# Optimization experiments

Hardware: AMD Instinct MI355X
Metric: run time of the kernel (lower is better)

## Reference

```python
import jax, jax.numpy as jnp
import numpy as np

DIM_E, DIM_M, DIM_C = 1024, 64, 128
B, N = 4, 4096


def setup_inputs() -> dict:
    key = jax.random.key(0)
    ks = jax.random.split(key, 10)
    s = 1.0 / np.sqrt(DIM_E + DIM_C)
    return {
        "e": jax.random.normal(ks[0], (B, N, DIM_E), jnp.float32),
        "m": jax.random.normal(ks[1], (B, N, DIM_M), jnp.float32),
        "c": jax.random.normal(ks[2], (B, N, DIM_C), jnp.float32),
        "l": jax.random.uniform(ks[3], (B, N), jnp.float32),
        "Wq": jax.random.uniform(ks[4], (DIM_E + DIM_C, DIM_E), jnp.float32, -s, s),
        "bq": jax.random.uniform(ks[5], (DIM_E,), jnp.float32, -s, s),
        "Wk": jax.random.uniform(ks[6], (DIM_E + DIM_C, DIM_E), jnp.float32, -s, s),
        "bk": jax.random.uniform(ks[7], (DIM_E,), jnp.float32, -s, s),
        "Wv": jax.random.uniform(ks[8], (DIM_E + DIM_C, DIM_E), jnp.float32, -s, s),
        "bv": jax.random.uniform(ks[9], (DIM_E,), jnp.float32, -s, s),
    }


def reference(e, m, c, l, Wq, bq, Wk, bk, Wv, bv):
    x = jnp.concatenate([e, c], axis=-1)                       # [B,N,De+Dc]
    q = jnp.einsum('bnd,df->bnf', x, Wq) + bq                  # [B,N,De]
    k = jnp.einsum('bnd,df->bnf', x, Wk) + bk
    v = jnp.einsum('bnd,df->bnf', x, Wv) + bv
    scale = 1.0 / jnp.sqrt(jnp.asarray(q.shape[-1], q.dtype))
    attn_scores = jnp.einsum('bqd,bkd->bqk', q, k) * scale     # [B,N,N]
    membrane_mask = jnp.einsum('bqm,bkm->bqk', m, m)           # [B,N,N]
    lifespan_mask = l[:, :, None] * l[:, None, :]              # [B,N,N]
    adaptive_scores = attn_scores * membrane_mask * lifespan_mask
    attn_weights = jax.nn.softmax(adaptive_scores, axis=-1)
    h_tilde = jnp.einsum('bqk,bkd->bqd', attn_weights, v)      # [B,N,De]
    e_new = e + h_tilde
    return (e_new, h_tilde)
```

## Files before the change

kernel.cpp:

```cpp
#include <hip/hip_runtime.h>
#include <hip/hip_bf16.h>

#define DE 1024
#define DM 64
#define DC 128
#define DX 1152
#define NB 4
#define NN 4096
#define NT 16384

typedef _Float16 f16;
typedef _Float16 f16x4 __attribute__((ext_vector_type(4)));
typedef _Float16 f16x8 __attribute__((ext_vector_type(8)));
typedef float f32x4 __attribute__((ext_vector_type(4)));

__device__ __forceinline__ void g2l16(const void* g, void* l) {
  __builtin_amdgcn_global_load_lds(
      (const __attribute__((address_space(1))) unsigned int*)(unsigned long long)g,
      (__attribute__((address_space(3))) unsigned int*)(unsigned int)(unsigned long long)l,
      16, 0, 0);
}

__global__ void build_x_kernel(const float* __restrict__ e, const float* __restrict__ c,
                               f16* __restrict__ Xb) {
  const int total = NT * DX / 4;
  for (int i = blockIdx.x * blockDim.x + threadIdx.x; i < total; i += gridDim.x * blockDim.x) {
    int idx = i * 4;
    int r = idx / DX, col = idx - r * DX;
    float4 v;
    if (col < DE) v = *(const float4*)(e + (long)r * DE + col);
    else          v = *(const float4*)(c + (long)r * DC + (col - DE));
    f16x4 o = { (f16)v.x, (f16)v.y, (f16)v.z, (f16)v.w };
    *(f16x4*)(Xb + (long)idx) = o;
  }
}

__global__ void conv_f16_kernel(const float* __restrict__ in, f16* __restrict__ out, int total4) {
  for (int i = blockIdx.x * blockDim.x + threadIdx.x; i < total4; i += gridDim.x * blockDim.x) {
    float4 v = *(const float4*)(in + (long)i * 4);
    f16x4 o = { (f16)v.x, (f16)v.y, (f16)v.z, (f16)v.w };
    *(f16x4*)(out + (long)i * 4) = o;
  }
}

__global__ void transpose_w_kernel(const float* __restrict__ in, f16* __restrict__ out) {
  __shared__ float tile[32][33];
  int c0 = blockIdx.x * 32, r0 = blockIdx.y * 32;
  int x = threadIdx.x, y = threadIdx.y;
#pragma unroll
  for (int i = 0; i < 4; ++i)
    tile[y + 8 * i][x] = in[(long)(r0 + y + 8 * i) * DE + (c0 + x)];
  __syncthreads();
#pragma unroll
  for (int i = 0; i < 4; ++i)
    out[(long)(c0 + y + 8 * i) * DX + (r0 + x)] = (f16)tile[x][y + 8 * i];
}

__device__ __forceinline__ void mm_loop(const f16* __restrict__ A, const f16* __restrict__ B,
                                        int lda, int ldb, int K,
                                        f16* lA, f16* lB, f32x4 (&acc)[4][4]) {
  const int t = threadIdx.x;
  const int lane = t & 63;
  const int wid = t >> 6;
  const int wr = (wid >> 1) * 64, wc = (wid & 1) * 64;
  const int fr = lane & 15, fq = lane >> 4;
  for (int k0 = 0; k0 < K; k0 += 32) {
    __syncthreads();
#pragma unroll
    for (int it = 0; it < 2; ++it) {
      int byteoff = it * 4096 + t * 16;
      int row = byteoff >> 6;
      int ke = (byteoff & 63) >> 1;
      g2l16(A + (long)row * lda + k0 + ke, lA + (byteoff >> 1));
      g2l16(B + (long)row * ldb + k0 + ke, lB + (byteoff >> 1));
    }
    __syncthreads();
    f16x8 af[4], bfr[4];
#pragma unroll
    for (int i = 0; i < 4; ++i) {
      af[i]  = *(const f16x8*)(lA + (wr + i * 16 + fr) * 32 + fq * 8);
      bfr[i] = *(const f16x8*)(lB + (wc + i * 16 + fr) * 32 + fq * 8);
    }
#pragma unroll
    for (int m = 0; m < 4; ++m)
#pragma unroll
      for (int n = 0; n < 4; ++n)
        acc[m][n] = __builtin_amdgcn_mfma_f32_16x16x32_f16(af[m], bfr[n], acc[m][n], 0, 0, 0);
  }
}

#define GEMM_PRE()                                                    \
  __shared__ __attribute__((aligned(16))) f16 lA[128 * 32], lB[128 * 32]; \
  f32x4 acc[4][4];                                                    \
  _Pragma("unroll") for (int m = 0; m < 4; ++m)                       \
  _Pragma("unroll") for (int n = 0; n < 4; ++n)                       \
      acc[m][n] = (f32x4){0.f, 0.f, 0.f, 0.f};

#define EPI_IDX()                                                     \
  const int lane = threadIdx.x & 63, wid = threadIdx.x >> 6;          \
  const int wr = (wid >> 1) * 64, wc = (wid & 1) * 64;                \
  const int fr = lane & 15, fq = lane >> 4;

__global__ __launch_bounds__(256) void gemm_qk_kernel(
    const f16* __restrict__ Xb, const f16* __restrict__ Wt,
    const float* __restrict__ bq, const float* __restrict__ bk,
    f16* __restrict__ qb, f16* __restrict__ kb) {
  GEMM_PRE();
  const int row0 = blockIdx.x * 128, col0 = blockIdx.y * 128;
  mm_loop(Xb + (long)row0 * DX, Wt + (long)col0 * DX, DX, DX, DX, lA, lB, acc);
  EPI_IDX();
#pragma unroll
  for (int n = 0; n < 4; ++n) {
    int col = col0 + wc + n * 16 + fr;
    float bias = (col < DE) ? bq[col] : bk[col - DE];
    f16* op = (col < DE) ? (qb + col) : (kb + col - DE);
#pragma unroll
    for (int m = 0; m < 4; ++m)
#pragma unroll
      for (int r = 0; r < 4; ++r) {
        int row = row0 + wr + m * 16 + fq * 4 + r;
        op[(long)row * DE] = (f16)(acc[m][n][r] + bias);
      }
  }
}

__global__ __launch_bounds__(256) void gemm_vt_kernel(
    const f16* __restrict__ WtV, const f16* __restrict__ Xb,
    const float* __restrict__ bv, f16* __restrict__ Vt) {
  GEMM_PRE();
  const int row0 = blockIdx.x * 128, col0 = blockIdx.y * 128;
  mm_loop(WtV + (long)row0 * DX, Xb + (long)col0 * DX, DX, DX, DX, lA, lB, acc);
  EPI_IDX();
#pragma unroll
  for (int n = 0; n < 4; ++n) {
    int col = col0 + wc + n * 16 + fr;
#pragma unroll
    for (int m = 0; m < 4; ++m)
#pragma unroll
      for (int r = 0; r < 4; ++r) {
        int row = row0 + wr + m * 16 + fq * 4 + r;
        Vt[(long)row * NT + col] = (f16)(acc[m][n][r] + bv[row]);
      }
  }
}

__global__ __launch_bounds__(256) void gemm_scores_kernel(
    const f16* __restrict__ qb, const f16* __restrict__ kb,
    const f16* __restrict__ mb, const float* __restrict__ l,
    float* __restrict__ S) {
  __shared__ __attribute__((aligned(16))) f16 lA[128 * 32], lB[128 * 32];
  f32x4 acc[4][4], am[4][4];
#pragma unroll
  for (int m = 0; m < 4; ++m)
#pragma unroll
    for (int n = 0; n < 4; ++n) {
      acc[m][n] = (f32x4){0.f, 0.f, 0.f, 0.f};
      am[m][n] = (f32x4){0.f, 0.f, 0.f, 0.f};
    }
  const int row0 = blockIdx.x * 128, col0 = blockIdx.y * 128;
  mm_loop(qb + (long)row0 * DE, kb + (long)col0 * DE, DE, DE, DE, lA, lB, acc);
  mm_loop(mb + (long)row0 * DM, mb + (long)col0 * DM, DM, DM, DM, lA, lB, am);
  EPI_IDX();
  const float scale = 0.03125f;
#pragma unroll
  for (int n = 0; n < 4; ++n) {
    int col = col0 + wc + n * 16 + fr;
    float lc = l[col];
#pragma unroll
    for (int m = 0; m < 4; ++m)
#pragma unroll
      for (int r = 0; r < 4; ++r) {
        int row = row0 + wr + m * 16 + fq * 4 + r;
        S[(long)row * NN + col] = acc[m][n][r] * scale * am[m][n][r] * l[row] * lc;
      }
  }
}

__global__ __launch_bounds__(256) void softmax_kernel(const float* __restrict__ S,
                                                      f16* __restrict__ P) {
  __shared__ float red[8];
  const long row = blockIdx.x;
  const float* s = S + row * NN;
  const int t = threadIdx.x;
  float4 v[4];
  float mx = -3.0e38f;
#pragma unroll
  for (int i = 0; i < 4; ++i) {
    v[i] = *(const float4*)(s + t * 4 + i * 1024);
    mx = fmaxf(mx, fmaxf(fmaxf(v[i].x, v[i].y), fmaxf(v[i].z, v[i].w)));
  }
#pragma unroll
  for (int o = 32; o; o >>= 1) mx = fmaxf(mx, __shfl_xor(mx, o));
  if ((t & 63) == 0) red[t >> 6] = mx;
  __syncthreads();
  mx = fmaxf(fmaxf(red[0], red[1]), fmaxf(red[2], red[3]));
  float sum = 0.f;
#pragma unroll
  for (int i = 0; i < 4; ++i) {
    v[i].x = __expf(v[i].x - mx); v[i].y = __expf(v[i].y - mx);
    v[i].z = __expf(v[i].z - mx); v[i].w = __expf(v[i].w - mx);
    sum += v[i].x + v[i].y + v[i].z + v[i].w;
  }
#pragma unroll
  for (int o = 32; o; o >>= 1) sum += __shfl_xor(sum, o);
  if ((t & 63) == 0) red[4 + (t >> 6)] = sum;
  __syncthreads();
  float inv = 1.f / (red[4] + red[5] + red[6] + red[7]);
  f16* p = P + row * NN;
#pragma unroll
  for (int i = 0; i < 4; ++i) {
    f16x4 o4 = { (f16)(v[i].x * inv), (f16)(v[i].y * inv),
                 (f16)(v[i].z * inv), (f16)(v[i].w * inv) };
    *(f16x4*)(p + t * 4 + i * 1024) = o4;
  }
}

__global__ __launch_bounds__(256) void gemm_pv_kernel(
    const f16* __restrict__ P, const f16* __restrict__ Vt,
    const float* __restrict__ e, float* __restrict__ outE, float* __restrict__ outH) {
  GEMM_PRE();
  const int b = blockIdx.z;
  const int row0 = blockIdx.x * 128, col0 = blockIdx.y * 128;
  const f16* A = P + (long)b * NN * NN + (long)row0 * NN;
  const f16* B = Vt + (long)col0 * NT + (long)b * NN;
  mm_loop(A, B, NN, NT, NN, lA, lB, acc);
  EPI_IDX();
#pragma unroll
  for (int n = 0; n < 4; ++n) {
    int col = col0 + wc + n * 16 + fr;
#pragma unroll
    for (int m = 0; m < 4; ++m)
#pragma unroll
      for (int r = 0; r < 4; ++r) {
        int row = row0 + wr + m * 16 + fq * 4 + r;
        long idx = ((long)b * NN + row) * DE + col;
        float h = acc[m][n][r];
        outE[idx] = e[idx] + h;
        outH[idx] = h;
      }
  }
}

extern "C" void kernel_launch(void* const* d_in, const int* in_sizes, int n_in,
                              void* d_out, int out_size, void* d_ws, size_t ws_size,
                              hipStream_t stream) {
  const float* e  = (const float*)d_in[0];
  const float* m  = (const float*)d_in[1];
  const float* c  = (const float*)d_in[2];
  const float* l  = (const float*)d_in[3];
  const float* Wq = (const float*)d_in[4];
  const float* bq = (const float*)d_in[5];
  const float* Wk = (const float*)d_in[6];
  const float* bk = (const float*)d_in[7];
  const float* Wv = (const float*)d_in[8];
  const float* bv = (const float*)d_in[9];
  float* outE = (float*)d_out;
  float* outH = outE + (long)NT * DE;

  char* ws = (char*)d_ws;
  size_t off = 0;
  auto alloc = [&](size_t bytes) {
    char* p = ws + off;
    off += (bytes + 255) & ~(size_t)255;
    return p;
  };
  f16* Xb    = (f16*)alloc((size_t)NT * DX * 2);
  f16* WtQK  = (f16*)alloc((size_t)2048 * DX * 2);
  f16* WtV   = (f16*)alloc((size_t)DE * DX * 2);
  f16* qb    = (f16*)alloc((size_t)NT * DE * 2);
  f16* kb    = (f16*)alloc((size_t)NT * DE * 2);
  f16* Vt    = (f16*)alloc((size_t)DE * NT * 2);
  f16* mb    = (f16*)alloc((size_t)NT * DM * 2);
  float* S   = (float*)alloc((size_t)NN * NN * 4);
  f16* P     = (f16*)alloc((size_t)NB * NN * NN * 2);
  if (off > ws_size) return;

  build_x_kernel<<<2048, 256, 0, stream>>>(e, c, Xb);
  conv_f16_kernel<<<512, 256, 0, stream>>>(m, mb, NT * DM / 4);
  transpose_w_kernel<<<dim3(32, 36), dim3(32, 8), 0, stream>>>(Wq, WtQK);
  transpose_w_kernel<<<dim3(32, 36), dim3(32, 8), 0, stream>>>(Wk, WtQK + (size_t)DE * DX);
  transpose_w_kernel<<<dim3(32, 36), dim3(32, 8), 0, stream>>>(Wv, WtV);
  gemm_qk_kernel<<<dim3(128, 16), 256, 0, stream>>>(Xb, WtQK, bq, bk, qb, kb);
  gemm_vt_kernel<<<dim3(8, 128), 256, 0, stream>>>(WtV, Xb, bv, Vt);
  for (int b = 0; b < NB; ++b) {
    gemm_scores_kernel<<<dim3(32, 32), 256, 0, stream>>>(
        qb + (size_t)b * NN * DE, kb + (size_t)b * NN * DE,
        mb + (size_t)b * NN * DM, l + (size_t)b * NN, S);
    softmax_kernel<<<NN, 256, 0, stream>>>(S, P + (size_t)b * NN * NN);
  }
  gemm_pv_kernel<<<dim3(32, 8, NB), 256, 0, stream>>>(P, Vt, e, outE, outH);
}
```

Before: 797.6 us.

## Replace GEMMs with 256x256 double-buffered swizzled MFMA core and precomputed mask

All four GEMMs (QK projection, V projection, scores, PV) move to a new 512-thread core with 256x256 tiles. The core uses 64-wide K steps, double-buffered XOR-swizzled LDS staged via global_load_lds, interleaved barriers with MFMA priority, and a grid swizzle. The membrane and lifespan mask is computed once per batch into the P buffer as fp16 with the scale folded in, and the softmax multiplies it in before normalising. The goal is more data reuse and better MFMA utilisation. The cost is 128KB of LDS per block, which limits occupancy, and some precision loss from storing the mask in fp16.

New measurement: 676.5 us. -15.2%, faster.

```diff
diff --git a/kernel.cpp b/kernel.cpp
--- a/kernel.cpp
+++ b/kernel.cpp
@@ -20,6 +20,9 @@
       (__attribute__((address_space(3))) unsigned int*)(unsigned int)(unsigned long long)l,
       16, 0, 0);
 }
+
+#define MEMF() asm volatile("" ::: "memory")
+#define BAR() { MEMF(); __builtin_amdgcn_s_barrier(); MEMF(); }
 
 __global__ void build_x_kernel(const float* __restrict__ e, const float* __restrict__ c,
                                f16* __restrict__ Xb) {
@@ -89,104 +92,288 @@
   }
 }
 
-#define GEMM_PRE()                                                    \
-  __shared__ __attribute__((aligned(16))) f16 lA[128 * 32], lB[128 * 32]; \
-  f32x4 acc[4][4];                                                    \
-  _Pragma("unroll") for (int m = 0; m < 4; ++m)                       \
-  _Pragma("unroll") for (int n = 0; n < 4; ++n)                       \
-      acc[m][n] = (f32x4){0.f, 0.f, 0.f, 0.f};
-
-#define EPI_IDX()                                                     \
-  const int lane = threadIdx.x & 63, wid = threadIdx.x >> 6;          \
-  const int wr = (wid >> 1) * 64, wc = (wid & 1) * 64;                \
+__global__ __launch_bounds__(256) void mask_kernel(
+    const f16* __restrict__ mb, const float* __restrict__ l, f16* __restrict__ Pm) {
+  __shared__ __attribute__((aligned(16))) f16 lA[128 * 32], lB[128 * 32];
+  f32x4 acc[4][4];
+#pragma unroll
+  for (int m = 0; m < 4; ++m)
+#pragma unroll
+    for (int n = 0; n < 4; ++n) acc[m][n] = (f32x4){0.f, 0.f, 0.f, 0.f};
+  const int b = blockIdx.z;
+  const int row0 = blockIdx.x * 128, col0 = blockIdx.y * 128;
+  mm_loop(mb + (long)(b * NN + row0) * DM, mb + (long)(b * NN + col0) * DM,
+          DM, DM, DM, lA, lB, acc);
+  const int lane = threadIdx.x & 63, wid = threadIdx.x >> 6;
+  const int wr = (wid >> 1) * 64, wc = (wid & 1) * 64;
   const int fr = lane & 15, fq = lane >> 4;
-
-__global__ __launch_bounds__(256) void gemm_qk_kernel(
+  const float* lb = l + (long)b * NN;
+  f16* out = Pm + (long)b * NN * NN;
+#pragma unroll
+  for (int n = 0; n < 4; ++n) {
+    int col = col0 + wc + n * 16 + fr;
+    float lc = lb[col] * 0.03125f;
+#pragma unroll
+    for (int m = 0; m < 4; ++m)
+#pragma unroll
+      for (int r = 0; r < 4; ++r) {
+        int row = row0 + wr + m * 16 + fq * 4 + r;
+        out[(long)row * NN + col] = (f16)(acc[m][n][r] * lc * lb[row]);
+      }
+  }
+}
+
+__device__ __forceinline__ void gemm8_core(
+    const f16* __restrict__ A, long lda,
+    const f16* __restrict__ B, long ldb,
+    int NTt, char* ldsb, f32x4 (&acc)[8][4]) {
+  const int tid = threadIdx.x;
+  const int lane = tid & 63, wid = tid >> 6;
+  const int wr = wid >> 2, wc = wid & 3;
+  const int fr = lane & 15, fq = lane >> 4;
+  const int cb0 = ((fq) ^ (fr & 7)) << 4;
+  const int cb1 = ((4 | fq) ^ (fr & 7)) << 4;
+
+  auto stageA = [&](int pc, int kt, int par) {
+    char* base = ldsb + par * 32768;
+    int k0 = kt * 64;
+#pragma unroll
+    for (int it = 0; it < 2; ++it) {
+      int p = it * 8192 + tid * 16;
+      int off = pc * 8192 + ((p >> 13) << 14) + (p & 8191);
+      int sw = off ^ (((off >> 7) & 7) << 4);
+      int row = sw >> 7;
+      int colf = ((sw >> 4) & 7) << 3;
+      g2l16(A + (long)row * lda + k0 + colf, base + off);
+    }
+  };
+  auto stageB = [&](int pc, int kt, int par) {
+    char* base = ldsb + 65536 + par * 32768;
+    int k0 = kt * 64;
+#pragma unroll
+    for (int it = 0; it < 2; ++it) {
+      int p = it * 8192 + tid * 16;
+      int off = pc * 4096 + ((p >> 12) << 13) + (p & 4095);
+      int sw = off ^ (((off >> 7) & 7) << 4);
+      int row = sw >> 7;
+      int colf = ((sw >> 4) & 7) << 3;
+      g2l16(B + (long)row * ldb + k0 + colf, base + off);
+    }
+  };
+
+  f16x8 af[4][2], bf0[2][2], bf1[2][2];
+  auto rdA = [&](int mh, int par) {
+    const char* base = ldsb + par * 32768;
+#pragma unroll
+    for (int i = 0; i < 4; ++i) {
+      int row = wr * 128 + mh * 64 + i * 16 + fr;
+      af[i][0] = *(const f16x8*)(const void*)(base + row * 128 + cb0);
+      af[i][1] = *(const f16x8*)(const void*)(base + row * 128 + cb1);
+    }
+  };
+  auto rdB = [&](f16x8 (&bf)[2][2], int nh, int par) {
+    const char* base = ldsb + 65536 + par * 32768;
+#pragma unroll
+    for (int i = 0; i < 2; ++i) {
+      int row = wc * 64 + nh * 32 + i * 16 + fr;
+      bf[i][0] = *(const f16x8*)(const void*)(base + row * 128 + cb0);
+      bf[i][1] = *(const f16x8*)(const void*)(base + row * 128 + cb1);
+    }
+  };
+  auto mma = [&](f16x8 (&bf)[2][2], int mo, int no) {
+    __builtin_amdgcn_s_setprio(1);
+#pragma unroll
+    for (int m = 0; m < 4; ++m)
+#pragma unroll
+      for (int n = 0; n < 2; ++n)
+#pragma unroll
+        for (int k = 0; k < 2; ++k)
+          acc[mo + m][no + n] =
+              __builtin_amdgcn_mfma_f32_16x16x32_f16(af[m][k], bf[n][k], acc[mo + m][no + n], 0, 0, 0);
+    __builtin_amdgcn_s_setprio(0);
+  };
+
+  MEMF();
+  stageA(0, 0, 0); stageB(0, 0, 0); stageA(1, 0, 0); stageB(1, 0, 0);
+  stageA(0, 1, 1); stageB(0, 1, 1); stageA(1, 1, 1);
+  asm volatile("s_waitcnt vmcnt(6)" ::: "memory");
+  BAR();
+
+  for (int t = 0; t < NTt; t += 2) {
+#pragma unroll
+    for (int half = 0; half < 2; ++half) {
+      const int tt = t + half;
+      const int par = half, npar = half ^ 1;
+      rdA(0, par); rdB(bf0, 0, par);
+      if (tt + 1 < NTt) stageB(1, tt + 1, npar);
+      BAR();
+      mma(bf0, 0, 0);
+      BAR();
+      rdB(bf1, 1, par);
+      if (tt + 2 < NTt) stageA(0, tt + 2, par);
+      BAR();
+      mma(bf1, 0, 2);
+      BAR();
+      rdA(1, par);
+      if (tt + 2 < NTt) stageB(0, tt + 2, par);
+      BAR();
+      mma(bf1, 4, 2);
+      BAR();
+      if (tt + 2 < NTt) stageA(1, tt + 2, par);
+      BAR();
+      mma(bf0, 4, 0);
+      if (tt + 1 < NTt) {
+        if (tt + 1 == NTt - 1) { asm volatile("s_waitcnt vmcnt(0)" ::: "memory"); }
+        else                   { asm volatile("s_waitcnt vmcnt(6)" ::: "memory"); }
+      }
+      BAR();
+    }
+  }
+  MEMF();
+}
+
+__device__ __forceinline__ void swz_grid(int& bx, int& by, int& bz) {
+  int nx = gridDim.x, ny = gridDim.y;
+  int flat = blockIdx.x + nx * (blockIdx.y + ny * blockIdx.z);
+  int total = nx * ny * gridDim.z;
+  int cpx = total >> 3;
+  flat = (flat & 7) * cpx + (flat >> 3);
+  bx = flat % nx; int r = flat / nx;
+  by = r % ny; bz = r / ny;
+}
+
+#define ACC_INIT()                                                  \
+  f32x4 acc[8][4];                                                  \
+  _Pragma("unroll") for (int m_ = 0; m_ < 8; ++m_)                  \
+  _Pragma("unroll") for (int n_ = 0; n_ < 4; ++n_)                  \
+      acc[m_][n_] = (f32x4){0.f, 0.f, 0.f, 0.f};
+
+#define EPI8_IDX()                                                  \
+  const int lane = threadIdx.x & 63, wid = threadIdx.x >> 6;        \
+  const int wr = wid >> 2, wc = wid & 3;                            \
+  const int fr = lane & 15, fq = lane >> 4;
+
+__global__ __launch_bounds__(512, 2) void qk8_kernel(
     const f16* __restrict__ Xb, const f16* __restrict__ Wt,
     const float* __restrict__ bq, const float* __restrict__ bk,
     f16* __restrict__ qb, f16* __restrict__ kb) {
-  GEMM_PRE();
-  const int row0 = blockIdx.x * 128, col0 = blockIdx.y * 128;
-  mm_loop(Xb + (long)row0 * DX, Wt + (long)col0 * DX, DX, DX, DX, lA, lB, acc);
-  EPI_IDX();
+  __shared__ __attribute__((aligned(128))) char ldsb[131072];
+  int bx, by, bz; swz_grid(bx, by, bz);
+  const int row0 = bx * 256, col0 = by * 256;
+  ACC_INIT();
+  gemm8_core(Xb + (long)row0 * DX, DX, Wt + (long)col0 * DX, DX, DX / 64, ldsb, acc);
+  EPI8_IDX();
+  const bool isq = col0 < DE;
+  const float* bvec = isq ? bq : bk;
+  f16* ob = isq ? qb : kb;
+  const int cbase = (isq ? col0 : col0 - DE) + wc * 64;
+  const int rbase = row0 + wr * 128;
 #pragma unroll
   for (int n = 0; n < 4; ++n) {
-    int col = col0 + wc + n * 16 + fr;
-    float bias = (col < DE) ? bq[col] : bk[col - DE];
-    f16* op = (col < DE) ? (qb + col) : (kb + col - DE);
-#pragma unroll
-    for (int m = 0; m < 4; ++m)
-#pragma unroll
-      for (int r = 0; r < 4; ++r) {
-        int row = row0 + wr + m * 16 + fq * 4 + r;
-        op[(long)row * DE] = (f16)(acc[m][n][r] + bias);
-      }
-  }
-}
-
-__global__ __launch_bounds__(256) void gemm_vt_kernel(
+    int col = cbase + n * 16 + fr;
+    float bb = bvec[col];
+#pragma unroll
+    for (int m = 0; m < 8; ++m)
+#pragma unroll
+      for (int j = 0; j < 4; ++j) {
+        int row = rbase + m * 16 + fq * 4 + j;
+        ob[(long)row * DE + col] = (f16)(acc[m][n][j] + bb);
+      }
+  }
+}
+
+__global__ __launch_bounds__(512, 2) void vt8_kernel(
     const f16* __restrict__ WtV, const f16* __restrict__ Xb,
     const float* __restrict__ bv, f16* __restrict__ Vt) {
-  GEMM_PRE();
-  const int row0 = blockIdx.x * 128, col0 = blockIdx.y * 128;
-  mm_loop(WtV + (long)row0 * DX, Xb + (long)col0 * DX, DX, DX, DX, lA, lB, acc);
-  EPI_IDX();
+  __shared__ __attribute__((aligned(128))) char ldsb[131072];
+  int bx, by, bz; swz_grid(bx, by, bz);
+  const int row0 = bx * 256, col0 = by * 256;
+  ACC_INIT();
+  gemm8_core(WtV + (long)row0 * DX, DX, Xb + (long)col0 * DX, DX, DX / 64, ldsb, acc);
+  EPI8_IDX();
+  const int cbase = col0 + wc * 64;
+  const int rbase = row0 + wr * 128;
 #pragma unroll
   for (int n = 0; n < 4; ++n) {
-    int col = col0 + wc + n * 16 + fr;
-#pragma unroll
-    for (int m = 0; m < 4; ++m)
-#pragma unroll
-      for (int r = 0; r < 4; ++r) {
-        int row = row0 + wr + m * 16 + fq * 4 + r;
-        Vt[(long)row * NT + col] = (f16)(acc[m][n][r] + bv[row]);
-      }
-  }
-}
-
-__global__ __launch_bounds__(256) void gemm_scores_kernel(
-    const f16* __restrict__ qb, const f16* __restrict__ kb,
-    const f16* __restrict__ mb, const float* __restrict__ l,
-    float* __restrict__ S) {
-  __shared__ __attribute__((aligned(16))) f16 lA[128 * 32], lB[128 * 32];
-  f32x4 acc[4][4], am[4][4];
-#pragma unroll
-  for (int m = 0; m < 4; ++m)
-#pragma unroll
-    for (int n = 0; n < 4; ++n) {
-      acc[m][n] = (f32x4){0.f, 0.f, 0.f, 0.f};
-      am[m][n] = (f32x4){0.f, 0.f, 0.f, 0.f};
-    }
-  const int row0 = blockIdx.x * 128, col0 = blockIdx.y * 128;
-  mm_loop(qb + (long)row0 * DE, kb + (long)col0 * DE, DE, DE, DE, lA, lB, acc);
-  mm_loop(mb + (long)row0 * DM, mb + (long)col0 * DM, DM, DM, DM, lA, lB, am);
-  EPI_IDX();
-  const float scale = 0.03125f;
+    int col = cbase + n * 16 + fr;
+#pragma unroll
+    for (int m = 0; m < 8; ++m)
+#pragma unroll
+      for (int j = 0; j < 4; ++j) {
+        int row = rbase + m * 16 + fq * 4 + j;
+        Vt[(long)row * NT + col] = (f16)(acc[m][n][j] + bv[row]);
+      }
+  }
+}
+
+__global__ __launch_bounds__(512, 2) void sc8_kernel(
+    const f16* __restrict__ qb_, const f16* __restrict__ kb_, float* __restrict__ S) {
+  __shared__ __attribute__((aligned(128))) char ldsb[131072];
+  int bx, by, bz; swz_grid(bx, by, bz);
+  const int row0 = bx * 256, col0 = by * 256;
+  ACC_INIT();
+  gemm8_core(qb_ + (long)row0 * DE, DE, kb_ + (long)col0 * DE, DE, DE / 64, ldsb, acc);
+  EPI8_IDX();
+  const int cbase = col0 + wc * 64;
+  const int rbase = row0 + wr * 128;
 #pragma unroll
   for (int n = 0; n < 4; ++n) {
-    int col = col0 + wc + n * 16 + fr;
-    float lc = l[col];
-#pragma unroll
-    for (int m = 0; m < 4; ++m)
-#pragma unroll
-      for (int r = 0; r < 4; ++r) {
-        int row = row0 + wr + m * 16 + fq * 4 + r;
-        S[(long)row * NN + col] = acc[m][n][r] * scale * am[m][n][r] * l[row] * lc;
+    int col = cbase + n * 16 + fr;
+#pragma unroll
+    for (int m = 0; m < 8; ++m)
+#pragma unroll
+      for (int j = 0; j < 4; ++j) {
+        int row = rbase + m * 16 + fq * 4 + j;
+        S[(long)row * NN + col] = acc[m][n][j];
+      }
+  }
+}
+
+__global__ __launch_bounds__(512, 2) void pv8_kernel(
+    const f16* __restrict__ P, const f16* __restrict__ Vt,
+    const float* __restrict__ e, float* __restrict__ outE, float* __restrict__ outH) {
+  __shared__ __attribute__((aligned(128))) char ldsb[131072];
+  int bx, by, bz; swz_grid(bx, by, bz);
+  const int b = bz;
+  const int row0 = bx * 256, col0 = by * 256;
+  ACC_INIT();
+  gemm8_core(P + (long)b * NN * NN + (long)row0 * NN, NN,
+             Vt + (long)col0 * NT + (long)b * NN, NT, NN / 64, ldsb, acc);
+  EPI8_IDX();
+  const int cbase = col0 + wc * 64;
+  const int rbase = row0 + wr * 128;
+#pragma unroll
+  for (int n = 0; n < 4; ++n) {
+    int col = cbase + n * 16 + fr;
+#pragma unroll
+    for (int m = 0; m < 8; ++m)
+#pragma unroll
+      for (int j = 0; j < 4; ++j) {
+        int row = rbase + m * 16 + fq * 4 + j;
+        long idx = ((long)b * NN + row) * DE + col;
+        float h = acc[m][n][j];
+        outE[idx] = e[idx] + h;
+        outH[idx] = h;
       }
   }
 }
 
 __global__ __launch_bounds__(256) void softmax_kernel(const float* __restrict__ S,
+                                                      const f16* __restrict__ Pm,
                                                       f16* __restrict__ P) {
   __shared__ float red[8];
   const long row = blockIdx.x;
   const float* s = S + row * NN;
+  const f16* pmr = Pm + row * NN;
   const int t = threadIdx.x;
   float4 v[4];
   float mx = -3.0e38f;
 #pragma unroll
   for (int i = 0; i < 4; ++i) {
     v[i] = *(const float4*)(s + t * 4 + i * 1024);
+    f16x4 m4 = *(const f16x4*)(pmr + t * 4 + i * 1024);
+    v[i].x *= (float)m4[0]; v[i].y *= (float)m4[1];
+    v[i].z *= (float)m4[2]; v[i].w *= (float)m4[3];
     mx = fmaxf(mx, fmaxf(fmaxf(v[i].x, v[i].y), fmaxf(v[i].z, v[i].w)));
   }
 #pragma unroll
@@ -212,32 +399,6 @@
     f16x4 o4 = { (f16)(v[i].x * inv), (f16)(v[i].y * inv),
                  (f16)(v[i].z * inv), (f16)(v[i].w * inv) };
     *(f16x4*)(p + t * 4 + i * 1024) = o4;
-  }
-}
-
-__global__ __launch_bounds__(256) void gemm_pv_kernel(
-    const f16* __restrict__ P, const f16* __restrict__ Vt,
-    const float* __restrict__ e, float* __restrict__ outE, float* __restrict__ outH) {
-  GEMM_PRE();
-  const int b = blockIdx.z;
-  const int row0 = blockIdx.x * 128, col0 = blockIdx.y * 128;
-  const f16* A = P + (long)b * NN * NN + (long)row0 * NN;
-  const f16* B = Vt + (long)col0 * NT + (long)b * NN;
-  mm_loop(A, B, NN, NT, NN, lA, lB, acc);
-  EPI_IDX();
-#pragma unroll
-  for (int n = 0; n < 4; ++n) {
-    int col = col0 + wc + n * 16 + fr;
-#pragma unroll
-    for (int m = 0; m < 4; ++m)
-#pragma unroll
-      for (int r = 0; r < 4; ++r) {
-        int row = row0 + wr + m * 16 + fq * 4 + r;
-        long idx = ((long)b * NN + row) * DE + col;
-        float h = acc[m][n][r];
-        outE[idx] = e[idx] + h;
-        outH[idx] = h;
-      }
   }
 }
 
@@ -280,13 +441,13 @@
   transpose_w_kernel<<<dim3(32, 36), dim3(32, 8), 0, stream>>>(Wq, WtQK);
   transpose_w_kernel<<<dim3(32, 36), dim3(32, 8), 0, stream>>>(Wk, WtQK + (size_t)DE * DX);
   transpose_w_kernel<<<dim3(32, 36), dim3(32, 8), 0, stream>>>(Wv, WtV);
-  gemm_qk_kernel<<<dim3(128, 16), 256, 0, stream>>>(Xb, WtQK, bq, bk, qb, kb);
-  gemm_vt_kernel<<<dim3(8, 128), 256, 0, stream>>>(WtV, Xb, bv, Vt);
+  mask_kernel<<<dim3(32, 32, NB), 256, 0, stream>>>(mb, l, P);
+  qk8_kernel<<<dim3(64, 8), 512, 0, stream>>>(Xb, WtQK, bq, bk, qb, kb);
+  vt8_kernel<<<dim3(4, 64), 512, 0, stream>>>(WtV, Xb, bv, Vt);
   for (int b = 0; b < NB; ++b) {
-    gemm_scores_kernel<<<dim3(32, 32), 256, 0, stream>>>(
-        qb + (size_t)b * NN * DE, kb + (size_t)b * NN * DE,
-        mb + (size_t)b * NN * DM, l + (size_t)b * NN, S);
-    softmax_kernel<<<NN, 256, 0, stream>>>(S, P + (size_t)b * NN * NN);
-  }
-  gemm_pv_kernel<<<dim3(32, 8, NB), 256, 0, stream>>>(P, Vt, e, outE, outH);
-}
+    sc8_kernel<<<dim3(16, 16), 512, 0, stream>>>(
+        qb + (size_t)b * NN * DE, kb + (size_t)b * NN * DE, S);
+    softmax_kernel<<<NN, 256, 0, stream>>>(S, P + (size_t)b * NN * NN, P + (size_t)b * NN * NN);
+  }
+  pv8_kernel<<<dim3(16, 4, NB), 512, 0, stream>>>(P, Vt, e, outE, outH);
+}
```
